# Performance work log

Hardware: AMD Instinct MI355X
Metric: run time of the kernel (lower is better)

## Reference

```python
import jax, jax.numpy as jnp
import numpy as np

BATCH, IN_DIM, GRID, HID, DEPTH = 2048, 128, 128, 256, 7
BN_EPS = 1e-5


def setup_inputs() -> dict:
    key = jax.random.key(0)
    ks = jax.random.split(key, 10)
    x = jax.random.uniform(ks[0], (BATCH, IN_DIM), dtype=jnp.float32)
    grids = jax.random.uniform(ks[1], (DEPTH, IN_DIM, GRID), dtype=jnp.float32)  # torch.rand init
    fs = jax.random.normal(ks[2], (DEPTH, IN_DIM, GRID, HID), dtype=jnp.float32)
    depth_scores = jnp.ones((DEPTH,), dtype=jnp.float32)
    mlp_W = jax.random.normal(ks[3], (3, HID, HID), dtype=jnp.float32) * (1.0 / np.sqrt(HID))
    mlp_b = jnp.zeros((3, HID), dtype=jnp.float32)
    bn_gamma = jnp.ones((3, HID), dtype=jnp.float32)
    bn_beta = jnp.zeros((3, HID), dtype=jnp.float32)
    W_out = jax.random.normal(ks[4], (HID, 1), dtype=jnp.float32) * (1.0 / np.sqrt(HID))
    b_out = jnp.zeros((1,), dtype=jnp.float32)
    return {"x": x, "grids": grids, "fs": fs, "depth_scores": depth_scores,
            "mlp_W": mlp_W, "mlp_b": mlp_b, "bn_gamma": bn_gamma,
            "bn_beta": bn_beta, "W_out": W_out, "b_out": b_out}


def reference(x, grids, fs, depth_scores, mlp_W, mlp_b, bn_gamma, bn_beta, W_out, b_out):
    # per-feature min-max normalization over the batch dim
    xmin = x.min(axis=0, keepdims=True)
    xmax = x.max(axis=0, keepdims=True)
    z = (x - xmin) / (xmax - xmin + 1e-6)  # [B, I]

    outputs = []
    for i in range(DEPTH):
        Bmat = jax.nn.relu(z[:, :, None] - grids[i][None, :, :])  # [B, I, G]
        # (B.unsqueeze(-1) * fs[i]).sum(2).sum(1) == einsum big,igh->bh
        H = jnp.einsum('big,igh->bh', Bmat, fs[i])  # [B, H]
        if i > 0:  # residual accumulation
            H = H + outputs[-1]
        outputs.append(H)
    stacked = jnp.stack(outputs, axis=0)  # [D, B, H]
    w = jax.nn.softmax(depth_scores)  # depth attention
    h = jnp.einsum('d,dbh->bh', w, stacked)

    # MLP head (BatchNorm uses batch stats = training-mode behaviour; Dropout off)
    for j in range(3):
        h = h @ mlp_W[j] + mlp_b[j]
        mean = h.mean(axis=0)
        var = h.var(axis=0)  # biased, matching torch BN normalization
        h = (h - mean) * jax.lax.rsqrt(var + BN_EPS) * bn_gamma[j] + bn_beta[j]
        h = jax.nn.gelu(h, approximate=False)  # torch nn.GELU is exact erf GELU
    return h @ W_out + b_out
```

## Files before the change

kernel.cpp:

```cpp
#include <hip/hip_runtime.h>
#include <hip/hip_bf16.h>

#define BATCH 2048
#define IN_DIM 128
#define GRIDN 128
#define HID 256
#define DEPTH 7

typedef unsigned int u32;
typedef __attribute__((ext_vector_type(8))) short short8;
typedef __attribute__((ext_vector_type(4))) float floatx4;

#define OFF_FST   ((size_t)0)
#define SZ_FST    ((size_t)7*128*256*128*2)
#define OFF_ZT    (OFF_FST + SZ_FST)
#define SZ_ZT     ((size_t)BATCH*IN_DIM*4)
#define OFF_HPRE  (OFF_ZT + SZ_ZT)
#define SZ_HPRE   ((size_t)BATCH*HID*4)
#define OFF_STATS (OFF_HPRE + SZ_HPRE)
#define SZ_STATS  ((size_t)3*2*HID*4)
#define OFF_KEYS  (OFF_STATS + SZ_STATS)
#define SZ_KEYS   ((size_t)256*4)
#define OFF_CW    (OFF_KEYS + SZ_KEYS)
#define SZ_CW     ((size_t)32)
#define OFF_Y1    (OFF_CW + SZ_CW)
#define SZ_Y      ((size_t)BATCH*HID*4)
#define OFF_Y2    (OFF_Y1 + SZ_Y)
#define OFF_Y3    (OFF_Y2 + SZ_Y)

#define FENCE __asm__ volatile("" ::: "memory")
#define WAITV(c) do { __builtin_amdgcn_s_waitcnt(c); FENCE; } while (0)
#define BARR do { FENCE; __builtin_amdgcn_s_barrier(); FENCE; } while (0)
#define VM8 0x0F78
#define VM4 0x0F74
#define VM0 0x0F70

__device__ __forceinline__ void gload_lds16(const void* g, void* l) {
  __builtin_amdgcn_global_load_lds(
      (const __attribute__((address_space(1))) u32*)g,
      (__attribute__((address_space(3))) u32*)l, 16, 0, 0);
}

__device__ __forceinline__ u32 pack2_bf16(float lo, float hi) {
  __hip_bfloat162 b2;
  b2.x = __float2bfloat16(lo);
  b2.y = __float2bfloat16(hi);
  return *reinterpret_cast<u32*>(&b2);
}

__device__ __forceinline__ u32 pk_trunc(float a, float b) {
  return __builtin_amdgcn_perm(__float_as_uint(b), __float_as_uint(a), 0x07060302u);
}

__device__ __forceinline__ float reluc(float v) {
  return __builtin_amdgcn_fmed3f(v, 0.0f, 1.0f);
}

__device__ __forceinline__ float gelu_exact(float x) {
  return 0.5f * x * (1.0f + erff(x * 0.70710678118654752f));
}

__global__ void convert_prep1_kernel(const float* __restrict__ fs,
                                     const float* __restrict__ depth_scores,
                                     const float* __restrict__ x,
                                     u32* __restrict__ keys,
                                     __hip_bfloat16* __restrict__ fs2) {
  __shared__ __align__(16) float lds3[3 * 16 * 256];
  int bid = blockIdx.x;
  int t = threadIdx.x;

  if (bid >= DEPTH * IN_DIM) {
    int pb = bid - DEPTH * IN_DIM;
    int base = pb * 256 + t;
    float mn = 1e30f, mx = -1e30f;
#pragma unroll
    for (int j = 0; j < 16; ++j) {
      float v = x[base + j * 16384];
      mn = fminf(mn, v); mx = fmaxf(mx, v);
    }
    float* smn = lds3; float* smx = lds3 + 256;
    smn[t] = mn; smx[t] = mx;
    __syncthreads();
    if (t < 128) {
      mn = fminf(smn[t], smn[t + 128]);
      mx = fmaxf(smx[t], smx[t + 128]);
      int i = base & 127;
      atomicMax(&keys[i], 0x7FFFFFFFu - __float_as_uint(mn));
      atomicMax(&keys[128 + i], __float_as_uint(mx));
    }
    return;
  }

  int slab = bid;
  int w = t >> 6, l = t & 63;
  int d = slab >> 7;
  float m = -1e30f; float ds[DEPTH];
#pragma unroll
  for (int i = 0; i < DEPTH; ++i) { ds[i] = depth_scores[i]; m = fmaxf(m, ds[i]); }
  float sum = 0.f, tail = 0.f;
#pragma unroll
  for (int i = 0; i < DEPTH; ++i) {
    float e = expf(ds[i] - m);
    sum += e;
    if (i >= d) tail += e;
  }
  float cd = tail / sum;

  const float* src = fs + (size_t)slab * (GRIDN * HID);
  char* dstb = (char*)fs2 + (size_t)slab * 65536;

  auto dmaPhase = [&](int p) {
    const float* s0 = src + (size_t)p * 16 * HID;
    char* bb = (char*)lds3 + (p % 3) * 16384;
#pragma unroll
    for (int i = 0; i < 4; ++i) {
      int sl = w * 4 + i;
      int r = p * 16 + sl;
      int mask = ((r >> 3) & 3) << 3;
      gload_lds16(s0 + (size_t)sl * HID + ((l * 4) ^ mask), bb + sl * 1024);
    }
  };
  auto packPhase = [&](int p) {
    int ks = p >> 1, hh = p & 1;
    const float* bb = lds3 + (p % 3) * 4096;
#pragma unroll
    for (int it = 0; it < 2; ++it) {
      int task = t + it * 256;
      int nhalf = task >> 8;
      int q = task & 255;
      int tt = q >> 5, l4h = (q >> 4) & 1, l15 = q & 15;
      int l4 = hh * 2 + l4h;
      int hgl = nhalf * 128 + tt * 16 + l15;
      int hx = hgl ^ (l4 << 3);
      const float* rp = bb + (l4h * 8) * 256 + hx;
      uint4 pk4;
      pk4.x = pack2_bf16(cd * rp[0 * 256], cd * rp[1 * 256]);
      pk4.y = pack2_bf16(cd * rp[2 * 256], cd * rp[3 * 256]);
      pk4.z = pack2_bf16(cd * rp[4 * 256], cd * rp[5 * 256]);
      pk4.w = pack2_bf16(cd * rp[6 * 256], cd * rp[7 * 256]);
      size_t off = (size_t)nhalf * 32768 + (size_t)ks * 8192 +
                   (size_t)tt * 1024 + (size_t)l4 * 256 + (size_t)l15 * 16;
      *(uint4*)(dstb + off) = pk4;
    }
  };

  dmaPhase(0); dmaPhase(1); FENCE;
#pragma unroll 1
  for (int p = 0; p < 6; ++p) {
    WAITV(VM4); BARR;
    dmaPhase(p + 2); FENCE;
    packPhase(p);
  }
  WAITV(VM4); BARR; packPhase(6);
  WAITV(VM0); BARR; packPhase(7);
}

__global__ void prep2_kernel(const float* __restrict__ x, const u32* __restrict__ keys,
                             float* __restrict__ z_t) {
  __shared__ float lds[128 * 65];
  int t = threadIdx.x;
  int b0 = blockIdx.x * 64;
#pragma unroll
  for (int q = 0; q < 32; ++q) {
    int idx = q * 256 + t;
    int b = idx >> 7, i = idx & 127;
    lds[i * 65 + b] = x[(size_t)(b0 + b) * IN_DIM + i];
  }
  __syncthreads();
#pragma unroll
  for (int q = 0; q < 32; ++q) {
    int idx = q * 256 + t;
    int ii = idx >> 6, bb = idx & 63;
    float mnv = __uint_as_float(0x7FFFFFFFu - keys[ii]);
    float mxv = __uint_as_float(keys[128 + ii]);
    float v = (lds[ii * 65 + bb] - mnv) * (1.0f / (mxv - mnv + 1e-6f));
    z_t[(size_t)ii * BATCH + b0 + bb] = v;
  }
}

__launch_bounds__(256, 2)
__global__ void gemm_kernel(const float* __restrict__ z_t,
                            const float* __restrict__ grids,
                            const __hip_bfloat16* __restrict__ fs2,
                            float* __restrict__ h_pre) {
  __shared__ __align__(16) char lds[24576];

  int bx = blockIdx.x;
  int xcd = bx & 7;
  int t6 = bx >> 3;
  int cg2 = t6 >> 4;
  int jb2 = t6 & 15;
  int chunk = xcd + 8 * cg2;
  int slab0 = chunk * 28;
  int mt = jb2 >> 1;
  int nh = jb2 & 1;

  int tid = threadIdx.x;
  int w = tid >> 6, l = tid & 63;
  int l15 = l & 15, l4 = l >> 4;
  int mbase = mt * 256 + w * 64;
  int nbase = nh * 128;

  floatx4 acc[4][8];
#pragma unroll
  for (int a = 0; a < 4; ++a)
#pragma unroll
    for (int b = 0; b < 8; ++b) acc[a][b] = (floatx4)0.f;

  const char* fsb = (const char*)fs2 + (size_t)slab0 * 65536 + (size_t)nh * 32768 +
                    (size_t)w * 2048 + (size_t)l * 16;

  auto stage8 = [&](int u, int bufIdx) {
    const char* srcb = fsb + (size_t)(u >> 2) * 65536 + (size_t)(u & 3) * 8192;
    char* dst = lds + bufIdx * 8192 + w * 2048;
    gload_lds16(srcb, dst);
    gload_lds16(srcb + 1024, dst + 1024);
  };

  float4 zA, zB;
  float4 g0A, g1A, g0B, g1B;
  auto zgload = [&](int s, float4& zv, float4& G0, float4& G1) {
    int slab = slab0 + (s >> 2);
    int iz = slab & 127;
    const float* zp = z_t + (size_t)iz * BATCH + mbase + l15;
    zv.x = zp[0]; zv.y = zp[16]; zv.z = zp[32]; zv.w = zp[48];
    const float* gp = grids + (size_t)slab * GRIDN + (s & 3) * 32 + l4 * 8;
    G0 = *(const float4*)gp;
    G1 = *(const float4*)(gp + 4);
  };

  short8 af[4];
  short8 bf[8];
  auto rdfrag8 = [&](int bufIdx) {
    const char* bp = lds + bufIdx * 8192 + l * 16;
#pragma unroll
    for (int tt = 0; tt < 8; ++tt)
      bf[tt] = *(const short8*)(bp + tt * 1024);
  };
  auto afgen = [&](const float4 zv, const float4 G0, const float4 G1) {
#pragma unroll
    for (int u = 0; u < 4; ++u) {
      float zu = (u == 0) ? zv.x : (u == 1) ? zv.y : (u == 2) ? zv.z : zv.w;
      union { uint4 q; short8 s8; } pk;
      pk.q.x = pk_trunc(reluc(zu - G0.x), reluc(zu - G0.y));
      pk.q.y = pk_trunc(reluc(zu - G0.z), reluc(zu - G0.w));
      pk.q.z = pk_trunc(reluc(zu - G1.x), reluc(zu - G1.y));
      pk.q.w = pk_trunc(reluc(zu - G1.z), reluc(zu - G1.w));
      af[u] = pk.s8;
    }
  };
  auto mfma32 = [&]() {
    __builtin_amdgcn_s_setprio(1);
#pragma unroll
    for (int u = 0; u < 4; ++u)
#pragma unroll
      for (int tt = 0; tt < 8; ++tt)
        acc[u][tt] = __builtin_amdgcn_mfma_f32_16x16x32_bf16(af[u], bf[tt], acc[u][tt], 0, 0, 0);
    __builtin_amdgcn_s_setprio(0);
  };

#define STEP_FULL(S, BUF, STBUF, ZV, G0, G1)                                   \
  do {                                                                         \
    WAITV(VM8); BARR;                                                          \
    stage8((S) + 2, (STBUF)); FENCE;                                           \
    rdfrag8(BUF);                                                              \
    afgen(ZV, G0, G1);                                                         \
    zgload((S) + 2, ZV, G0, G1); FENCE;                                        \
    mfma32();                                                                  \
  } while (0)

  stage8(0, 0); FENCE;
  zgload(0, zA, g0A, g1A); FENCE;
  stage8(1, 1); FENCE;
  zgload(1, zB, g0B, g1B); FENCE;

#pragma unroll 1
  for (int s0 = 0; s0 < 108; s0 += 6) {
    STEP_FULL(s0 + 0, 0, 2, zA, g0A, g1A);
    STEP_FULL(s0 + 1, 1, 0, zB, g0B, g1B);
    STEP_FULL(s0 + 2, 2, 1, zA, g0A, g1A);
    STEP_FULL(s0 + 3, 0, 2, zB, g0B, g1B);
    STEP_FULL(s0 + 4, 1, 0, zA, g0A, g1A);
    STEP_FULL(s0 + 5, 2, 1, zB, g0B, g1B);
  }

  STEP_FULL(108, 0, 2, zA, g0A, g1A);
  STEP_FULL(109, 1, 0, zB, g0B, g1B);
  WAITV(VM8); BARR;
  rdfrag8(2);
  afgen(zA, g0A, g1A);
  mfma32();
  WAITV(VM0); BARR;
  rdfrag8(0);
  afgen(zB, g0B, g1B);
  mfma32();

  int row0 = mbase + l4 * 4;
  int col0 = nbase + l15;
#pragma unroll
  for (int u = 0; u < 4; ++u) {
#pragma unroll
    for (int tt = 0; tt < 8; ++tt) {
      int col = col0 + tt * 16;
#pragma unroll
      for (int r = 0; r < 4; ++r) {
        int row = row0 + u * 16 + r;
        atomicAdd(&h_pre[(size_t)row * HID + col], acc[u][tt][r]);
      }
    }
  }
}

template <int FIRST>
__launch_bounds__(256, 2)
__global__ void mlp_kernel(const float* __restrict__ Xin,
                           const float* __restrict__ statsIn,
                           const float* __restrict__ gamma,
                           const float* __restrict__ beta,
                           const float* __restrict__ W,
                           const float* __restrict__ bias,
                           float* __restrict__ Yout,
                           float* __restrict__ statsOut) {
  __shared__ float Xs[4][HID];
  __shared__ __align__(16) float Wl[2][32][HID];
  int br = blockIdx.x, c = threadIdx.x;
  int w = c >> 6, l = c & 63;

  auto stageW = [&](int t, int buf) {
    const float* src = W + ((size_t)t * 32 + w * 8) * HID + l * 4;
#pragma unroll
    for (int i = 0; i < 8; ++i)
      gload_lds16(src + (size_t)i * HID, &Wl[buf][w * 8 + i][0]);
  };

  stageW(0, 0); FENCE;

  float mean = 0.f, rstd = 1.f, gm = 1.f, bt = 0.f;
  if (!FIRST) {
    float s1 = statsIn[c], s2 = statsIn[HID + c];
    mean = s1 * (1.0f / BATCH);
    float var = s2 * (1.0f / BATCH) - mean * mean;
    rstd = rsqrtf(var + 1e-5f);
    gm = gamma[c]; bt = beta[c];
  }
#pragma unroll
  for (int r = 0; r < 4; ++r) {
    float v = Xin[(size_t)(br * 4 + r) * HID + c];
    if (!FIRST) v = gelu_exact((v - mean) * rstd * gm + bt);
    Xs[r][c] = v;
  }
  __syncthreads();

  float acc[4] = {0.f, 0.f, 0.f, 0.f};
#pragma unroll 1
  for (int t = 0; t < 8; ++t) {
    if (t < 7) { stageW(t + 1, (t + 1) & 1); FENCE; }
    if (t < 7) { WAITV(VM8); } else { WAITV(VM0); }
    BARR;
    const float* wt = &Wl[t & 1][0][0];
    int kb = t * 32;
#pragma unroll 8
    for (int kk = 0; kk < 32; ++kk) {
      float wv = wt[kk * HID + c];
#pragma unroll
      for (int r = 0; r < 4; ++r) acc[r] += Xs[r][kb + kk] * wv;
    }
    BARR;
  }

  float bb = bias[c];
  float s1 = 0.f, s2 = 0.f;
#pragma unroll
  for (int r = 0; r < 4; ++r) {
    float y = acc[r] + bb;
    Yout[(size_t)(br * 4 + r) * HID + c] = y;
    s1 += y; s2 += y * y;
  }
  atomicAdd(&statsOut[c], s1);
  atomicAdd(&statsOut[HID + c], s2);
}

__global__ void final_kernel(const float* __restrict__ Y3,
                             const float* __restrict__ statsIn,
                             const float* __restrict__ gamma,
                             const float* __restrict__ beta,
                             const float* __restrict__ W_out,
                             const float* __restrict__ b_out,
                             float* __restrict__ out) {
  int w = threadIdx.x >> 6, l = threadIdx.x & 63;
  int b = blockIdx.x * 4 + w;
  float4 y = *(const float4*)(Y3 + (size_t)b * HID + l * 4);
  float4 wv = *(const float4*)(W_out + l * 4);
  float r4[4] = {y.x, y.y, y.z, y.w};
  float w4[4] = {wv.x, wv.y, wv.z, wv.w};
  float s = 0.f;
  int c0 = l * 4;
#pragma unroll
  for (int q = 0; q < 4; ++q) {
    int c = c0 + q;
    float s1 = statsIn[c], s2 = statsIn[HID + c];
    float mean = s1 * (1.0f / BATCH);
    float var = s2 * (1.0f / BATCH) - mean * mean;
    float rstd = rsqrtf(var + 1e-5f);
    float v = gelu_exact((r4[q] - mean) * rstd * gamma[c] + beta[c]);
    s += v * w4[q];
  }
#pragma unroll
  for (int off = 32; off > 0; off >>= 1) s += __shfl_down(s, off);
  if (l == 0) out[b] = s + b_out[0];
}

extern "C" void kernel_launch(void* const* d_in, const int* in_sizes, int n_in,
                              void* d_out, int out_size, void* d_ws, size_t ws_size,
                              hipStream_t stream) {
  const float* x      = (const float*)d_in[0];
  const float* grids  = (const float*)d_in[1];
  const float* fs     = (const float*)d_in[2];
  const float* dscore = (const float*)d_in[3];
  const float* mlp_W  = (const float*)d_in[4];
  const float* mlp_b  = (const float*)d_in[5];
  const float* bn_g   = (const float*)d_in[6];
  const float* bn_b   = (const float*)d_in[7];
  const float* W_out  = (const float*)d_in[8];
  const float* b_out  = (const float*)d_in[9];
  float* out = (float*)d_out;

  char* ws = (char*)d_ws;
  __hip_bfloat16* fs2 = (__hip_bfloat16*)(ws + OFF_FST);
  float* z_t   = (float*)(ws + OFF_ZT);
  float* h_pre = (float*)(ws + OFF_HPRE);
  float* stats = (float*)(ws + OFF_STATS);
  u32*   keys  = (u32*)(ws + OFF_KEYS);
  float* Y1    = (float*)(ws + OFF_Y1);
  float* Y2    = (float*)(ws + OFF_Y2);
  float* Y3    = (float*)(ws + OFF_Y3);

  hipMemsetAsync(h_pre, 0, SZ_HPRE + SZ_STATS + SZ_KEYS, stream);

  convert_prep1_kernel<<<DEPTH * IN_DIM + 64, 256, 0, stream>>>(fs, dscore, x,
                                                                keys, fs2);
  prep2_kernel<<<32, 256, 0, stream>>>(x, keys, z_t);
  gemm_kernel<<<512, 256, 0, stream>>>(z_t, grids, fs2, h_pre);

  mlp_kernel<1><<<512, 256, 0, stream>>>(h_pre, nullptr, nullptr, nullptr,
                                         mlp_W, mlp_b, Y1, stats);
  mlp_kernel<0><<<512, 256, 0, stream>>>(Y1, stats, bn_g, bn_b,
                                         mlp_W + 65536, mlp_b + 256, Y2, stats + 512);
  mlp_kernel<0><<<512, 256, 0, stream>>>(Y2, stats + 512, bn_g + 256, bn_b + 256,
                                         mlp_W + 2 * 65536, mlp_b + 2 * 256, Y3, stats + 1024);
  final_kernel<<<512, 256, 0, stream>>>(Y3, stats + 1024, bn_g + 512, bn_b + 512,
                                        W_out, b_out, out);
}
```

Measured before the change: 419.6 us.

## Switch main GEMM to 32x32x16 bf16 MFMA with matching fs layout

Replaces the 16x16x32 MFMA tiling in the gemm kernel with 32x32x16 bf16 MFMAs, which changes the accumulator shape, the A-fragment generation, the LDS B-fragment reads (now in two halves), and the atomic output mapping. The fs pre-pack kernel is rewritten to emit the packed bf16 layout expected by 32x32 fragments and drops the XOR swizzle on the DMA load. The larger MFMA tile is meant to give higher math throughput per instruction and fewer fragment loads. In exchange, the unswizzled LDS reads in the pack kernel may hit bank conflicts, and splitting the B reads into halves may change how well loads overlap with MFMAs.

```diff
diff --git a/kernel.cpp b/kernel.cpp
--- a/kernel.cpp
+++ b/kernel.cpp
@@ -10,6 +10,7 @@
 typedef unsigned int u32;
 typedef __attribute__((ext_vector_type(8))) short short8;
 typedef __attribute__((ext_vector_type(4))) float floatx4;
+typedef __attribute__((ext_vector_type(16))) float floatx16;
 
 #define OFF_FST   ((size_t)0)
 #define SZ_FST    ((size_t)7*128*256*128*2)
@@ -115,9 +116,7 @@
 #pragma unroll
     for (int i = 0; i < 4; ++i) {
       int sl = w * 4 + i;
-      int r = p * 16 + sl;
-      int mask = ((r >> 3) & 3) << 3;
-      gload_lds16(s0 + (size_t)sl * HID + ((l * 4) ^ mask), bb + sl * 1024);
+      gload_lds16(s0 + (size_t)sl * HID + l * 4, bb + sl * 1024);
     }
   };
   auto packPhase = [&](int p) {
@@ -126,20 +125,18 @@
 #pragma unroll
     for (int it = 0; it < 2; ++it) {
       int task = t + it * 256;
-      int nhalf = task >> 8;
+      int nh = task >> 8;
       int q = task & 255;
-      int tt = q >> 5, l4h = (q >> 4) & 1, l15 = q & 15;
-      int l4 = hh * 2 + l4h;
-      int hgl = nhalf * 128 + tt * 16 + l15;
-      int hx = hgl ^ (l4 << 3);
-      const float* rp = bb + (l4h * 8) * 256 + hx;
+      int v = q >> 6, lq = q & 63;
+      int h = nh * 128 + v * 32 + (lq & 31);
+      const float* rp = bb + ((lq >> 5) * 8) * 256 + h;
       uint4 pk4;
       pk4.x = pack2_bf16(cd * rp[0 * 256], cd * rp[1 * 256]);
       pk4.y = pack2_bf16(cd * rp[2 * 256], cd * rp[3 * 256]);
       pk4.z = pack2_bf16(cd * rp[4 * 256], cd * rp[5 * 256]);
       pk4.w = pack2_bf16(cd * rp[6 * 256], cd * rp[7 * 256]);
-      size_t off = (size_t)nhalf * 32768 + (size_t)ks * 8192 +
-                   (size_t)tt * 1024 + (size_t)l4 * 256 + (size_t)l15 * 16;
+      size_t off = (size_t)nh * 32768 + (size_t)ks * 8192 + (size_t)v * 2048 +
+                   (size_t)hh * 1024 + (size_t)lq * 16;
       *(uint4*)(dstb + off) = pk4;
     }
   };
@@ -197,15 +194,15 @@
 
   int tid = threadIdx.x;
   int w = tid >> 6, l = tid & 63;
-  int l15 = l & 15, l4 = l >> 4;
+  int l31 = l & 31, lhi = l >> 5;
   int mbase = mt * 256 + w * 64;
   int nbase = nh * 128;
 
-  floatx4 acc[4][8];
-#pragma unroll
-  for (int a = 0; a < 4; ++a)
-#pragma unroll
-    for (int b = 0; b < 8; ++b) acc[a][b] = (floatx4)0.f;
+  floatx16 acc[2][4];
+#pragma unroll
+  for (int a = 0; a < 2; ++a)
+#pragma unroll
+    for (int b = 0; b < 4; ++b) acc[a][b] = (floatx16)0.f;
 
   const char* fsb = (const char*)fs2 + (size_t)slab0 * 65536 + (size_t)nh * 32768 +
                     (size_t)w * 2048 + (size_t)l * 16;
@@ -217,95 +214,114 @@
     gload_lds16(srcb + 1024, dst + 1024);
   };
 
-  float4 zA, zB;
-  float4 g0A, g1A, g0B, g1B;
-  auto zgload = [&](int s, float4& zv, float4& G0, float4& G1) {
+  float zA0, zA1, zB0, zB1;
+  float4 gA0, gA0b, gA1, gA1b, gB0, gB0b, gB1, gB1b;
+  auto zgload = [&](int s, float& z0, float& z1, float4& G0, float4& G0b,
+                    float4& G1, float4& G1b) {
     int slab = slab0 + (s >> 2);
     int iz = slab & 127;
-    const float* zp = z_t + (size_t)iz * BATCH + mbase + l15;
-    zv.x = zp[0]; zv.y = zp[16]; zv.z = zp[32]; zv.w = zp[48];
-    const float* gp = grids + (size_t)slab * GRIDN + (s & 3) * 32 + l4 * 8;
+    const float* zp = z_t + (size_t)iz * BATCH + mbase + l31;
+    z0 = zp[0]; z1 = zp[32];
+    const float* gp = grids + (size_t)slab * GRIDN + (s & 3) * 32 + lhi * 8;
     G0 = *(const float4*)gp;
-    G1 = *(const float4*)(gp + 4);
+    G0b = *(const float4*)(gp + 4);
+    G1 = *(const float4*)(gp + 16);
+    G1b = *(const float4*)(gp + 20);
   };
 
   short8 af[4];
-  short8 bf[8];
-  auto rdfrag8 = [&](int bufIdx) {
-    const char* bp = lds + bufIdx * 8192 + l * 16;
-#pragma unroll
-    for (int tt = 0; tt < 8; ++tt)
-      bf[tt] = *(const short8*)(bp + tt * 1024);
-  };
-  auto afgen = [&](const float4 zv, const float4 G0, const float4 G1) {
-#pragma unroll
-    for (int u = 0; u < 4; ++u) {
-      float zu = (u == 0) ? zv.x : (u == 1) ? zv.y : (u == 2) ? zv.z : zv.w;
-      union { uint4 q; short8 s8; } pk;
-      pk.q.x = pk_trunc(reluc(zu - G0.x), reluc(zu - G0.y));
-      pk.q.y = pk_trunc(reluc(zu - G0.z), reluc(zu - G0.w));
-      pk.q.z = pk_trunc(reluc(zu - G1.x), reluc(zu - G1.y));
-      pk.q.w = pk_trunc(reluc(zu - G1.z), reluc(zu - G1.w));
-      af[u] = pk.s8;
-    }
-  };
-  auto mfma32 = [&]() {
+  short8 bf4[4];
+  auto rdhalf = [&](int bufIdx, int h2) {
+    const char* bp = lds + bufIdx * 8192 + (size_t)(h2 * 2) * 2048 + l * 16;
+    bf4[0] = *(const short8*)(bp);
+    bf4[1] = *(const short8*)(bp + 1024);
+    bf4[2] = *(const short8*)(bp + 2048);
+    bf4[3] = *(const short8*)(bp + 3072);
+  };
+  auto afgen = [&](float z0, float z1, const float4 G0, const float4 G0b,
+                   const float4 G1, const float4 G1b) {
+#pragma unroll
+    for (int u = 0; u < 2; ++u) {
+      float zu = u ? z1 : z0;
+      union { uint4 q; short8 s8; } p0, p1;
+      p0.q.x = pk_trunc(reluc(zu - G0.x), reluc(zu - G0.y));
+      p0.q.y = pk_trunc(reluc(zu - G0.z), reluc(zu - G0.w));
+      p0.q.z = pk_trunc(reluc(zu - G0b.x), reluc(zu - G0b.y));
+      p0.q.w = pk_trunc(reluc(zu - G0b.z), reluc(zu - G0b.w));
+      p1.q.x = pk_trunc(reluc(zu - G1.x), reluc(zu - G1.y));
+      p1.q.y = pk_trunc(reluc(zu - G1.z), reluc(zu - G1.w));
+      p1.q.z = pk_trunc(reluc(zu - G1b.x), reluc(zu - G1b.y));
+      p1.q.w = pk_trunc(reluc(zu - G1b.z), reluc(zu - G1b.w));
+      af[u * 2 + 0] = p0.s8;
+      af[u * 2 + 1] = p1.s8;
+    }
+  };
+  auto mfhalf = [&](int h2) {
     __builtin_amdgcn_s_setprio(1);
 #pragma unroll
-    for (int u = 0; u < 4; ++u)
-#pragma unroll
-      for (int tt = 0; tt < 8; ++tt)
-        acc[u][tt] = __builtin_amdgcn_mfma_f32_16x16x32_bf16(af[u], bf[tt], acc[u][tt], 0, 0, 0);
+    for (int u = 0; u < 2; ++u)
+#pragma unroll
+      for (int vv = 0; vv < 2; ++vv) {
+        int v = h2 * 2 + vv;
+        acc[u][v] = __builtin_amdgcn_mfma_f32_32x32x16_bf16(af[u * 2 + 0], bf4[vv * 2 + 0], acc[u][v], 0, 0, 0);
+        acc[u][v] = __builtin_amdgcn_mfma_f32_32x32x16_bf16(af[u * 2 + 1], bf4[vv * 2 + 1], acc[u][v], 0, 0, 0);
+      }
     __builtin_amdgcn_s_setprio(0);
   };
 
-#define STEP_FULL(S, BUF, STBUF, ZV, G0, G1)                                   \
+#define STEP_FULL(S, BUF, STBUF, Z0, Z1, G0, G0b, G1, G1b)                     \
   do {                                                                         \
     WAITV(VM8); BARR;                                                          \
     stage8((S) + 2, (STBUF)); FENCE;                                           \
-    rdfrag8(BUF);                                                              \
-    afgen(ZV, G0, G1);                                                         \
-    zgload((S) + 2, ZV, G0, G1); FENCE;                                        \
-    mfma32();                                                                  \
+    rdhalf(BUF, 0);                                                            \
+    afgen(Z0, Z1, G0, G0b, G1, G1b);                                           \
+    zgload((S) + 2, Z0, Z1, G0, G0b, G1, G1b); FENCE;                          \
+    mfhalf(0);                                                                 \
+    rdhalf(BUF, 1);                                                            \
+    mfhalf(1);                                                                 \
   } while (0)
 
   stage8(0, 0); FENCE;
-  zgload(0, zA, g0A, g1A); FENCE;
+  zgload(0, zA0, zA1, gA0, gA0b, gA1, gA1b); FENCE;
   stage8(1, 1); FENCE;
-  zgload(1, zB, g0B, g1B); FENCE;
+  zgload(1, zB0, zB1, gB0, gB0b, gB1, gB1b); FENCE;
 
 #pragma unroll 1
   for (int s0 = 0; s0 < 108; s0 += 6) {
-    STEP_FULL(s0 + 0, 0, 2, zA, g0A, g1A);
-    STEP_FULL(s0 + 1, 1, 0, zB, g0B, g1B);
-    STEP_FULL(s0 + 2, 2, 1, zA, g0A, g1A);
-    STEP_FULL(s0 + 3, 0, 2, zB, g0B, g1B);
-    STEP_FULL(s0 + 4, 1, 0, zA, g0A, g1A);
-    STEP_FULL(s0 + 5, 2, 1, zB, g0B, g1B);
-  }
-
-  STEP_FULL(108, 0, 2, zA, g0A, g1A);
-  STEP_FULL(109, 1, 0, zB, g0B, g1B);
+    STEP_FULL(s0 + 0, 0, 2, zA0, zA1, gA0, gA0b, gA1, gA1b);
+    STEP_FULL(s0 + 1, 1, 0, zB0, zB1, gB0, gB0b, gB1, gB1b);
+    STEP_FULL(s0 + 2, 2, 1, zA0, zA1, gA0, gA0b, gA1, gA1b);
+    STEP_FULL(s0 + 3, 0, 2, zB0, zB1, gB0, gB0b, gB1, gB1b);
+    STEP_FULL(s0 + 4, 1, 0, zA0, zA1, gA0, gA0b, gA1, gA1b);
+    STEP_FULL(s0 + 5, 2, 1, zB0, zB1, gB0, gB0b, gB1, gB1b);
+  }
+
+  STEP_FULL(108, 0, 2, zA0, zA1, gA0, gA0b, gA1, gA1b);
+  STEP_FULL(109, 1, 0, zB0, zB1, gB0, gB0b, gB1, gB1b);
   WAITV(VM8); BARR;
-  rdfrag8(2);
-  afgen(zA, g0A, g1A);
-  mfma32();
+  rdhalf(2, 0);
+  afgen(zA0, zA1, gA0, gA0b, gA1, gA1b);
+  mfhalf(0);
+  rdhalf(2, 1);
+  mfhalf(1);
   WAITV(VM0); BARR;
-  rdfrag8(0);
-  afgen(zB, g0B, g1B);
-  mfma32();
-
-  int row0 = mbase + l4 * 4;
-  int col0 = nbase + l15;
-#pragma unroll
-  for (int u = 0; u < 4; ++u) {
-#pragma unroll
-    for (int tt = 0; tt < 8; ++tt) {
-      int col = col0 + tt * 16;
-#pragma unroll
-      for (int r = 0; r < 4; ++r) {
-        int row = row0 + u * 16 + r;
-        atomicAdd(&h_pre[(size_t)row * HID + col], acc[u][tt][r]);
+  rdhalf(0, 0);
+  afgen(zB0, zB1, gB0, gB0b, gB1, gB1b);
+  mfhalf(0);
+  rdhalf(0, 1);
+  mfhalf(1);
+
+  int colb = nbase + l31;
+  int rowb = mbase + 4 * lhi;
+#pragma unroll
+  for (int u = 0; u < 2; ++u) {
+#pragma unroll
+    for (int v = 0; v < 4; ++v) {
+      int col = colb + v * 32;
+#pragma unroll
+      for (int r = 0; r < 16; ++r) {
+        int row = rowb + u * 32 + (r & 3) + 8 * (r >> 2);
+        atomicAdd(&h_pre[(size_t)row * HID + col], acc[u][v][r]);
       }
     }
   }
```

Result: slower. 436.6 us (+4.0%).
